# Performance work log

Hardware: AMD Instinct MI355X
Metric: run time of the kernel (lower is better)

The kernel has to match this reference:

```python
import jax, jax.numpy as jnp
import numpy as np

N_EMBED = 40
HEAD_SIZE = 10
N_HEADS = 4
LN_EPS = 1e-5


def _layernorm(x, g, b):
    mu = jnp.mean(x, axis=-1, keepdims=True)
    var = jnp.mean(jnp.square(x - mu), axis=-1, keepdims=True)
    return (x - mu) * jax.lax.rsqrt(var + LN_EPS) * g + b


def setup_inputs() -> dict:
    key = jax.random.key(0)
    ks = jax.random.split(key, 12)
    B, T = 16, 2048
    s = 1.0 / np.sqrt(N_EMBED)
    return {
        "x": jax.random.normal(ks[0], (B, T, N_EMBED), dtype=jnp.float32),
        # per-head Q/K/V weights stacked: [H, n_embed, head_size]
        "Wq": jax.random.normal(ks[1], (N_HEADS, N_EMBED, HEAD_SIZE), dtype=jnp.float32) * s,
        "Wk": jax.random.normal(ks[2], (N_HEADS, N_EMBED, HEAD_SIZE), dtype=jnp.float32) * s,
        "Wv": jax.random.normal(ks[3], (N_HEADS, N_EMBED, HEAD_SIZE), dtype=jnp.float32) * s,
        "Wp": jax.random.normal(ks[4], (N_EMBED, N_EMBED), dtype=jnp.float32) * s,
        "bp": jnp.zeros((N_EMBED,), dtype=jnp.float32),
        "W1": jax.random.normal(ks[5], (N_EMBED, N_EMBED), dtype=jnp.float32) * s,
        "b1": jnp.zeros((N_EMBED,), dtype=jnp.float32),
        "W2": jax.random.normal(ks[6], (N_EMBED, N_EMBED), dtype=jnp.float32) * s,
        "b2": jnp.zeros((N_EMBED,), dtype=jnp.float32),
        "g1": jnp.ones((N_EMBED,), dtype=jnp.float32),
        "be1": jnp.zeros((N_EMBED,), dtype=jnp.float32),
        "g2": jnp.ones((N_EMBED,), dtype=jnp.float32),
        "be2": jnp.zeros((N_EMBED,), dtype=jnp.float32),
    }


def reference(x, Wq, Wk, Wv, Wp, bp, W1, b1, W2, b2, g1, be1, g2, be2):
    B, T, D = x.shape
    # --- pre-norm (note: original overwrites x, so residual uses ln1(x)) ---
    x = _layernorm(x, g1, be1)
    # --- multi-head attention (faithful to source: scores = k @ q^T, no scale, no mask) ---
    q = jnp.einsum("btd,hde->bhte", x, Wq)  # [B,H,T,hs]
    k = jnp.einsum("btd,hde->bhte", x, Wk)
    v = jnp.einsum("btd,hde->bhte", x, Wv)
    w = jnp.einsum("bhie,bhje->bhij", k, q)  # k @ q.transpose(-2,-1)
    w = jax.nn.softmax(w, axis=-1)
    out = jnp.einsum("bhij,bhje->bhie", w, v)  # [B,H,T,hs]
    out = jnp.transpose(out, (0, 2, 1, 3)).reshape(B, T, D)  # concat heads
    out = out @ Wp + bp
    x = x + out
    # --- second norm + FFN (residual uses ln2(x), as in source) ---
    x = _layernorm(x, g2, be2)
    h = jax.nn.relu(x @ W1 + b1)
    x = x + (h @ W2 + b2)
    return x
```

## Files before the change

kernel.cpp:

```cpp
#include <hip/hip_runtime.h>
#include <math.h>

namespace {

using bf16x8 = __attribute__((ext_vector_type(8))) short;
using f32x4  = __attribute__((ext_vector_type(4))) float;

constexpr int D   = 40;
constexpr int HS  = 10;
constexpr int NH  = 4;
constexpr int TT  = 2048;
constexpr int BB  = 16;
constexpr int ROWS = BB * TT;
constexpr int PE  = 16;
constexpr int VR  = 11;
constexpr float LOG2E = 1.4426950408889634f;

__device__ inline unsigned short f2b(float x) {
    unsigned int u = __float_as_uint(x);
    unsigned int r = (u + 0x7fffu + ((u >> 16) & 1u)) >> 16;
    return (unsigned short)r;
}

__device__ inline f32x4 mfma32(bf16x8 a, bf16x8 b, f32x4 c) {
    return __builtin_amdgcn_mfma_f32_16x16x32_bf16(a, b, c, 0, 0, 0);
}

__device__ inline float dot40(const float* __restrict__ xr,
                              const float* __restrict__ w) {
    float s0 = 0.f, s1 = 0.f, s2 = 0.f, s3 = 0.f;
    const float4* w4 = reinterpret_cast<const float4*>(w);
    #pragma unroll
    for (int i = 0; i < 10; ++i) {
        float4 t = w4[i];
        s0 = fmaf(xr[4*i+0], t.x, s0);
        s1 = fmaf(xr[4*i+1], t.y, s1);
        s2 = fmaf(xr[4*i+2], t.z, s2);
        s3 = fmaf(xr[4*i+3], t.w, s3);
    }
    return (s0 + s1) + (s2 + s3);
}

__global__ __launch_bounds__(256) void k_ln_qkv(
    const float* __restrict__ x,  const float* __restrict__ Wq,
    const float* __restrict__ Wk, const float* __restrict__ Wv,
    const float* __restrict__ g1, const float* __restrict__ be1,
    float* __restrict__ xn, unsigned short* __restrict__ qb,
    unsigned short* __restrict__ kb, unsigned short* __restrict__ vT)
{
    __shared__ float wt_s[3*NH*HS*D];
    __shared__ float g_s[D], b_s[D];
    const int tid = threadIdx.x;
    for (int i = tid; i < NH*D*HS; i += 256) {
        const int h = i / (D*HS), r = i % (D*HS);
        const int d = r / HS, e = r % HS;
        const int to = (h*HS + e)*D + d;
        wt_s[to]              = Wq[i];
        wt_s[NH*HS*D + to]    = Wk[i];
        wt_s[2*NH*HS*D + to]  = Wv[i];
    }
    if (tid < D) { g_s[tid] = g1[tid]; b_s[tid] = be1[tid]; }
    __syncthreads();

    const int gid = blockIdx.x * 256 + tid;
    const int eh  = gid & 1;
    const int h   = (gid >> 1) & 3;
    const int row = gid >> 3;

    float xr[D];
    const float4* xp = reinterpret_cast<const float4*>(x + (size_t)row * D);
    #pragma unroll
    for (int i = 0; i < D/4; ++i) {
        float4 t4 = xp[i];
        xr[4*i+0]=t4.x; xr[4*i+1]=t4.y; xr[4*i+2]=t4.z; xr[4*i+3]=t4.w;
    }
    float mu = 0.f;
    #pragma unroll
    for (int d = 0; d < D; ++d) mu += xr[d];
    mu *= (1.f/D);
    float var = 0.f;
    #pragma unroll
    for (int d = 0; d < D; ++d) { float dd = xr[d]-mu; var += dd*dd; }
    var *= (1.f/D);
    const float rs = rsqrtf(var + 1e-5f);
    #pragma unroll
    for (int d = 0; d < D; ++d) xr[d] = (xr[d]-mu)*rs*g_s[d] + b_s[d];

    if ((gid & 7) == 0) {
        float4* xo = reinterpret_cast<float4*>(xn + (size_t)row * D);
        #pragma unroll
        for (int i = 0; i < D/4; ++i) {
            float4 t4; t4.x=xr[4*i+0]; t4.y=xr[4*i+1]; t4.z=xr[4*i+2]; t4.w=xr[4*i+3];
            xo[i] = t4;
        }
    }

    const int b = row >> 11;
    const int t = row & (TT-1);
    const int bh = b*NH + h;
    const int e0 = eh * 5;

    float aq[5], ak[5], av[5];
    #pragma unroll
    for (int e = 0; e < 5; ++e) {
        aq[e] = dot40(xr, &wt_s[(h*HS + e0 + e)*D]);
        ak[e] = dot40(xr, &wt_s[NH*HS*D + (h*HS + e0 + e)*D]);
        av[e] = dot40(xr, &wt_s[2*NH*HS*D + (h*HS + e0 + e)*D]);
    }

    float send[5], recv[5];
    #pragma unroll
    for (int j = 0; j < 5; ++j) send[j] = eh ? aq[j] : ak[j];
    #pragma unroll
    for (int j = 0; j < 5; ++j) recv[j] = __shfl_xor(send[j], 1);

    const float scale = eh ? 1.f : LOG2E;
    float lo[5], hi[5];
    #pragma unroll
    for (int j = 0; j < 5; ++j) {
        lo[j] = eh ? recv[j] : aq[j];
        hi[j] = eh ? ak[j]   : recv[j];
    }
    union { unsigned short u[PE]; uint4 v4[2]; } U;
    #pragma unroll
    for (int e = 0; e < PE; ++e)
        U.u[e] = (e < 5) ? f2b(lo[e]*scale)
               : (e < 10) ? f2b(hi[e-5]*scale) : (unsigned short)0;
    unsigned short* dst = (eh ? kb : qb) + ((size_t)bh*TT + t)*PE;
    uint4* d4 = reinterpret_cast<uint4*>(dst);
    d4[0] = U.v4[0]; d4[1] = U.v4[1];

    #pragma unroll
    for (int e = 0; e < 5; ++e)
        vT[((size_t)bh*VR + e0 + e)*TT + t] = f2b(av[e]);
    if (eh) vT[((size_t)bh*VR + HS)*TT + t] = 0x3F80;
}

__global__ __launch_bounds__(256, 4) void k_attn(
    const unsigned short* __restrict__ qb, const unsigned short* __restrict__ kb,
    const unsigned short* __restrict__ vT, float* __restrict__ ao)
{
    __shared__ __align__(16) unsigned short PT[4][16][40];
    const int w    = threadIdx.x >> 6;
    const int lane = threadIdx.x & 63;
    const int g    = lane >> 4;
    const int li   = lane & 15;
    const int bh   = blockIdx.y;
    const int i0   = blockIdx.x * 64 + w * 16;
    const size_t bT = (size_t)bh * TT;

    const bf16x8 zero8 = {0,0,0,0,0,0,0,0};
    const f32x4  zacc  = {0.f,0.f,0.f,0.f};

    bf16x8 kf = zero8;
    if (g < 2) kf = *reinterpret_cast<const bf16x8*>(kb + (bT + i0 + li)*PE + 8*g);

    f32x4 acc = zacc;
    const unsigned short* vrow = vT + ((size_t)bh*VR + (li <= HS ? li : 0))*TT;

    #pragma unroll 2
    for (int jt = 0; jt < TT; jt += 32) {
        bf16x8 a0 = zero8, a1 = zero8;
        if (g < 2) {
            a0 = *reinterpret_cast<const bf16x8*>(qb + (bT + jt      + li)*PE + 8*g);
            a1 = *reinterpret_cast<const bf16x8*>(qb + (bT + jt + 16 + li)*PE + 8*g);
        }
        f32x4 s0 = __builtin_amdgcn_mfma_f32_16x16x32_bf16(a0, kf, zacc, 0, 0, 0);
        f32x4 s1 = __builtin_amdgcn_mfma_f32_16x16x32_bf16(a1, kf, zacc, 0, 0, 0);

        const float p0 = __builtin_amdgcn_exp2f(s0[0]), p1 = __builtin_amdgcn_exp2f(s0[1]);
        const float p2 = __builtin_amdgcn_exp2f(s0[2]), p3 = __builtin_amdgcn_exp2f(s0[3]);
        const float p4 = __builtin_amdgcn_exp2f(s1[0]), p5 = __builtin_amdgcn_exp2f(s1[1]);
        const float p6 = __builtin_amdgcn_exp2f(s1[2]), p7 = __builtin_amdgcn_exp2f(s1[3]);

        unsigned int w0, w1, w2, w3;
        asm("v_cvt_pk_bf16_f32 %0, %1, %2" : "=v"(w0) : "v"(p0), "v"(p1));
        asm("v_cvt_pk_bf16_f32 %0, %1, %2" : "=v"(w1) : "v"(p2), "v"(p3));
        asm("v_cvt_pk_bf16_f32 %0, %1, %2" : "=v"(w2) : "v"(p4), "v"(p5));
        asm("v_cvt_pk_bf16_f32 %0, %1, %2" : "=v"(w3) : "v"(p6), "v"(p7));
        *reinterpret_cast<uint2*>(&PT[w][li][4*g])      = make_uint2(w0, w1);
        *reinterpret_cast<uint2*>(&PT[w][li][16 + 4*g]) = make_uint2(w2, w3);

        bf16x8 pf = *reinterpret_cast<const bf16x8*>(&PT[w][li][8*g]);
        bf16x8 vf = zero8;
        if (li <= HS) vf = *reinterpret_cast<const bf16x8*>(vrow + jt + 8*g);
        acc = __builtin_amdgcn_mfma_f32_16x16x32_bf16(vf, pf, acc, 0, 0, 0);
    }

    const float l = __shfl(acc[2], 32 + li);
    const float linv = 1.f / l;
    float* orow = ao + (bT + i0 + li) * HS;
    #pragma unroll
    for (int r = 0; r < 4; ++r) {
        const int e = 4*g + r;
        if (e < HS) orow[e] = acc[r] * linv;
    }
}

__global__ __launch_bounds__(256) void k_epilogue(
    const float* __restrict__ attn, const float* __restrict__ xn,
    const float* __restrict__ Wp, const float* __restrict__ bp,
    const float* __restrict__ W1, const float* __restrict__ b1,
    const float* __restrict__ W2, const float* __restrict__ b2,
    const float* __restrict__ g2, const float* __restrict__ be2,
    float* __restrict__ out)
{
    __shared__ float wp_s[D*D], w1_s[D*D], w2_s[D*D];
    __shared__ float bp_s[D], b1_s[D], b2_s[D], g_s[D], be_s[D];
    const int tid = threadIdx.x;
    for (int i = tid; i < D*D; i += 256) { wp_s[i]=Wp[i]; w1_s[i]=W1[i]; w2_s[i]=W2[i]; }
    if (tid < D) {
        bp_s[tid]=bp[tid]; b1_s[tid]=b1[tid]; b2_s[tid]=b2[tid];
        g_s[tid]=g2[tid]; be_s[tid]=be2[tid];
    }
    __syncthreads();

    const int gid  = blockIdx.x * 256 + tid;
    const int row  = gid >> 2;
    const int q4   = gid & 3;
    const int b0   = q4 * 10;
    const int lane = tid & 63;
    const int base = lane & 60;
    const int b    = row >> 11;
    const int t    = row & (TT-1);

    float cat[D];
    #pragma unroll
    for (int h = 0; h < NH; ++h) {
        const float2* ap = reinterpret_cast<const float2*>(
            attn + ((((size_t)b*NH + h)*TT) + t)*HS);
        #pragma unroll
        for (int e = 0; e < HS/2; ++e) {
            float2 t2 = ap[e];
            cat[h*HS + 2*e] = t2.x; cat[h*HS + 2*e + 1] = t2.y;
        }
    }

    float y[10];
    {
        const float2* xp = reinterpret_cast<const float2*>(xn + (size_t)row*D + b0);
        #pragma unroll
        for (int i = 0; i < 5; ++i) {
            float2 t2 = xp[i];
            y[2*i+0] = t2.x; y[2*i+1] = t2.y;
        }
    }
    #pragma unroll
    for (int d = 0; d < 10; ++d) y[d] += bp_s[b0+d];
    for (int c = 0; c < D; ++c) {
        const float cc = cat[c];
        const float* wr = &wp_s[c*D + b0];
        #pragma unroll
        for (int d = 0; d < 10; ++d) y[d] = fmaf(cc, wr[d], y[d]);
    }

    float sp = 0.f;
    #pragma unroll
    for (int d = 0; d < 10; ++d) sp += y[d];
    sp += __shfl_xor(sp, 1); sp += __shfl_xor(sp, 2);
    const float mu = sp * (1.f/D);
    float vp = 0.f;
    #pragma unroll
    for (int d = 0; d < 10; ++d) { float dd = y[d]-mu; vp += dd*dd; }
    vp += __shfl_xor(vp, 1); vp += __shfl_xor(vp, 2);
    const float rs = rsqrtf(vp * (1.f/D) + 1e-5f);

    float y2[10];
    #pragma unroll
    for (int d = 0; d < 10; ++d) y2[d] = (y[d]-mu)*rs*g_s[b0+d] + be_s[b0+d];

    float z[D];
    #pragma unroll
    for (int seg = 0; seg < 4; ++seg)
        #pragma unroll
        for (int j = 0; j < 10; ++j)
            z[seg*10 + j] = __shfl(y2[j], base + seg);

    float hd[10];
    #pragma unroll
    for (int d = 0; d < 10; ++d) hd[d] = b1_s[b0+d];
    for (int c = 0; c < D; ++c) {
        const float cc = z[c];
        const float* wr = &w1_s[c*D + b0];
        #pragma unroll
        for (int d = 0; d < 10; ++d) hd[d] = fmaf(cc, wr[d], hd[d]);
    }
    #pragma unroll
    for (int d = 0; d < 10; ++d) hd[d] = fmaxf(hd[d], 0.f);

    float hf[D];
    #pragma unroll
    for (int seg = 0; seg < 4; ++seg)
        #pragma unroll
        for (int j = 0; j < 10; ++j)
            hf[seg*10 + j] = __shfl(hd[j], base + seg);

    float ov[10];
    #pragma unroll
    for (int d = 0; d < 10; ++d) ov[d] = y2[d] + b2_s[b0+d];
    for (int c = 0; c < D; ++c) {
        const float cc = hf[c];
        const float* wr = &w2_s[c*D + b0];
        #pragma unroll
        for (int d = 0; d < 10; ++d) ov[d] = fmaf(cc, wr[d], ov[d]);
    }

    float2* op = reinterpret_cast<float2*>(out + (size_t)row*D + b0);
    #pragma unroll
    for (int i = 0; i < 5; ++i) {
        float2 t2; t2.x = ov[2*i]; t2.y = ov[2*i+1];
        op[i] = t2;
    }
}

}

extern "C" void kernel_launch(void* const* d_in, const int* in_sizes, int n_in,
                              void* d_out, int out_size, void* d_ws, size_t ws_size,
                              hipStream_t stream) {
    const float* x   = (const float*)d_in[0];
    const float* Wq  = (const float*)d_in[1];
    const float* Wk  = (const float*)d_in[2];
    const float* Wv  = (const float*)d_in[3];
    const float* Wp  = (const float*)d_in[4];
    const float* bp  = (const float*)d_in[5];
    const float* W1  = (const float*)d_in[6];
    const float* b1  = (const float*)d_in[7];
    const float* W2  = (const float*)d_in[8];
    const float* b2  = (const float*)d_in[9];
    const float* g1  = (const float*)d_in[10];
    const float* be1 = (const float*)d_in[11];
    const float* g2  = (const float*)d_in[12];
    const float* be2 = (const float*)d_in[13];

    const size_t N = (size_t)ROWS * D;
    float* xn = (float*)d_ws;
    float* ao = xn + N;
    unsigned short* qb = (unsigned short*)(ao + N);
    unsigned short* kb = qb + (size_t)BB*NH*TT*PE;
    unsigned short* vT = kb + (size_t)BB*NH*TT*PE;

    k_ln_qkv<<<ROWS*8/256, 256, 0, stream>>>(x, Wq, Wk, Wv, g1, be1, xn, qb, kb, vT);
    k_attn<<<dim3(TT/64, BB*NH), 256, 0, stream>>>(qb, kb, vT, ao);
    k_epilogue<<<ROWS*4/256, 256, 0, stream>>>(ao, xn, Wp, bp, W1, b1, W2, b2, g2, be2,
                                               (float*)d_out);
}
```

Baseline: 113.5 us.

## Vectorize weight staging loads and add MFMA priority hints in attention loop

Weight staging into shared memory in the QKV and epilogue kernels now uses float4 global loads instead of scalar loads, cutting the number of load instructions in each block's prologue. The attention inner loop is unrolled 4 instead of 2, and s_setprio raises wave priority around the MFMA instructions so matrix issue is favoured over other waves. These are small prologue and scheduling tweaks. The larger unroll may raise register pressure and lower occupancy.

```diff
diff --git a/kernel.cpp b/kernel.cpp
--- a/kernel.cpp
+++ b/kernel.cpp
@@ -20,10 +20,6 @@
     unsigned int u = __float_as_uint(x);
     unsigned int r = (u + 0x7fffu + ((u >> 16) & 1u)) >> 16;
     return (unsigned short)r;
-}
-
-__device__ inline f32x4 mfma32(bf16x8 a, bf16x8 b, f32x4 c) {
-    return __builtin_amdgcn_mfma_f32_16x16x32_bf16(a, b, c, 0, 0, 0);
 }
 
 __device__ inline float dot40(const float* __restrict__ xr,
@@ -51,13 +47,26 @@
     __shared__ float wt_s[3*NH*HS*D];
     __shared__ float g_s[D], b_s[D];
     const int tid = threadIdx.x;
-    for (int i = tid; i < NH*D*HS; i += 256) {
-        const int h = i / (D*HS), r = i % (D*HS);
-        const int d = r / HS, e = r % HS;
-        const int to = (h*HS + e)*D + d;
-        wt_s[to]              = Wq[i];
-        wt_s[NH*HS*D + to]    = Wk[i];
-        wt_s[2*NH*HS*D + to]  = Wv[i];
+    {
+        const float4* Wq4 = reinterpret_cast<const float4*>(Wq);
+        const float4* Wk4 = reinterpret_cast<const float4*>(Wk);
+        const float4* Wv4 = reinterpret_cast<const float4*>(Wv);
+        for (int i4 = tid; i4 < NH*D*HS/4; i4 += 256) {
+            float4 qv = Wq4[i4], kv = Wk4[i4], vv = Wv4[i4];
+            const float* qf = reinterpret_cast<const float*>(&qv);
+            const float* kf = reinterpret_cast<const float*>(&kv);
+            const float* vf = reinterpret_cast<const float*>(&vv);
+            #pragma unroll
+            for (int c = 0; c < 4; ++c) {
+                const int i = i4*4 + c;
+                const int h = i / (D*HS), r = i % (D*HS);
+                const int d = r / HS, e = r % HS;
+                const int to = (h*HS + e)*D + d;
+                wt_s[to]              = qf[c];
+                wt_s[NH*HS*D + to]    = kf[c];
+                wt_s[2*NH*HS*D + to]  = vf[c];
+            }
+        }
     }
     if (tid < D) { g_s[tid] = g1[tid]; b_s[tid] = be1[tid]; }
     __syncthreads();
@@ -158,15 +167,17 @@
     f32x4 acc = zacc;
     const unsigned short* vrow = vT + ((size_t)bh*VR + (li <= HS ? li : 0))*TT;
 
-    #pragma unroll 2
+    #pragma unroll 4
     for (int jt = 0; jt < TT; jt += 32) {
         bf16x8 a0 = zero8, a1 = zero8;
         if (g < 2) {
             a0 = *reinterpret_cast<const bf16x8*>(qb + (bT + jt      + li)*PE + 8*g);
             a1 = *reinterpret_cast<const bf16x8*>(qb + (bT + jt + 16 + li)*PE + 8*g);
         }
+        __builtin_amdgcn_s_setprio(1);
         f32x4 s0 = __builtin_amdgcn_mfma_f32_16x16x32_bf16(a0, kf, zacc, 0, 0, 0);
         f32x4 s1 = __builtin_amdgcn_mfma_f32_16x16x32_bf16(a1, kf, zacc, 0, 0, 0);
+        __builtin_amdgcn_s_setprio(0);
 
         const float p0 = __builtin_amdgcn_exp2f(s0[0]), p1 = __builtin_amdgcn_exp2f(s0[1]);
         const float p2 = __builtin_amdgcn_exp2f(s0[2]), p3 = __builtin_amdgcn_exp2f(s0[3]);
@@ -184,7 +195,9 @@
         bf16x8 pf = *reinterpret_cast<const bf16x8*>(&PT[w][li][8*g]);
         bf16x8 vf = zero8;
         if (li <= HS) vf = *reinterpret_cast<const bf16x8*>(vrow + jt + 8*g);
+        __builtin_amdgcn_s_setprio(1);
         acc = __builtin_amdgcn_mfma_f32_16x16x32_bf16(vf, pf, acc, 0, 0, 0);
+        __builtin_amdgcn_s_setprio(0);
     }
 
     const float l = __shfl(acc[2], 32 + li);
@@ -208,7 +221,17 @@
     __shared__ float wp_s[D*D], w1_s[D*D], w2_s[D*D];
     __shared__ float bp_s[D], b1_s[D], b2_s[D], g_s[D], be_s[D];
     const int tid = threadIdx.x;
-    for (int i = tid; i < D*D; i += 256) { wp_s[i]=Wp[i]; w1_s[i]=W1[i]; w2_s[i]=W2[i]; }
+    {
+        float4* wp4 = reinterpret_cast<float4*>(wp_s);
+        float4* w14 = reinterpret_cast<float4*>(w1_s);
+        float4* w24 = reinterpret_cast<float4*>(w2_s);
+        const float4* Wp4 = reinterpret_cast<const float4*>(Wp);
+        const float4* W14 = reinterpret_cast<const float4*>(W1);
+        const float4* W24 = reinterpret_cast<const float4*>(W2);
+        for (int i = tid; i < D*D/4; i += 256) {
+            wp4[i] = Wp4[i]; w14[i] = W14[i]; w24[i] = W24[i];
+        }
+    }
     if (tid < D) {
         bp_s[tid]=bp[tid]; b1_s[tid]=b1[tid]; b2_s[tid]=b2[tid];
         g_s[tid]=g2[tid]; be_s[tid]=be2[tid];
```

After: 110.0 us, median of 3. -3.1%, faster.
